# Performance work log

Measured on AMD Instinct MI355X. Metric: run time of the kernel, lower is better.

The kernel has to match this reference:

```python
import jax, jax.numpy as jnp
import numpy as np
from jax.scipy.linalg import solve_triangular

LS = 0.5414            # frozen GP length scale (_gp_scale.data = 0.5414)
L2 = LS * LS
D = 2
K_OPS = D + 2          # operators: identity, d/dx_i (i=1..d), laplacian
JITTER_KXX = 1e-5
JITTER_AKA = 1e-4
JITTER_YY = 1e-5


def _opiK(xout, xin, l2, d):
    # op_i applied to first arg of RBF kernel -> (bs, k, m, n)
    r = xout[:, :, None, :] - xin[:, None, :, :]            # (bs,m,n,d)
    u = jnp.sum(r * r, axis=-1) / l2                        # (bs,m,n)
    K = jnp.exp(-0.5 * u)
    ri = jnp.moveaxis(r, -1, 1)                             # (bs,d,m,n)
    grad = -(ri / l2) * K[:, None]                          # d/dx_i K
    lap = ((u - d) / l2) * K                                # Lap_x K
    return jnp.concatenate([K[:, None], grad, lap[:, None]], axis=1)


def _opiKopjfull(x, l2, d):
    # op_i on first arg, op_j on second arg -> (bs, k, k, m, m)
    r = x[:, :, None, :] - x[:, None, :, :]
    u = jnp.sum(r * r, axis=-1) / l2
    K = jnp.exp(-0.5 * u)
    ri = jnp.moveaxis(r, -1, 1)                             # (bs,d,m,m)
    gK = (ri / l2) * K[:, None]                             # d/dy_j K
    lapK = ((u - d) / l2) * K                               # Lap K (either arg)
    eye = jnp.eye(d, dtype=x.dtype)[None, :, :, None, None]
    gg = (eye / l2 - ri[:, :, None] * ri[:, None] / (l2 * l2)) * K[:, None, None]  # d/dx_i d/dy_j K
    glap = (ri / (l2 * l2)) * (((2.0 + d - u) * K)[:, None])  # d/dx_i Lap_y K
    laplap = (((u - d) ** 2 - 4.0 * u + 2.0 * d) / (l2 * l2)) * K  # Lap_x Lap_y K
    row0 = jnp.concatenate([K[:, None, None], gK[:, None], lapK[:, None, None]], axis=2)
    rowg = jnp.concatenate([(-gK)[:, :, None], gg, glap[:, :, None]], axis=2)
    rowl = jnp.concatenate([lapK[:, None, None], (-glap)[:, None], laplap[:, None, None]], axis=2)
    return jnp.concatenate([row0, rowg, rowl], axis=1)


def _psd_solve(L, B):
    # (Kxx + jitter I)^{-1} B via Cholesky (stands in for gpytorch inv_matmul/CG)
    y = solve_triangular(L, B, lower=True)
    return solve_triangular(L, y, lower=True, trans=1)


def _forward(xin, meanin, Kin, weight, bias):
    bs, n, c = meanin.shape
    d, k, l2 = D, K_OPS, L2
    xout, m = xin, n
    r = xin[:, :, None, :] - xin[:, None, :, :]
    Kxx = jnp.exp(-0.5 * jnp.sum(r * r, axis=-1) / l2)      # (bs,n,n)
    In = jnp.eye(n, dtype=xin.dtype)
    Lc = jnp.linalg.cholesky(Kxx + JITTER_KXX * In)
    opiKmn = _opiK(xout, xin, l2, d)                        # (bs,k,m,n)
    # posterior mean of op_i applied to the GP
    opimean = (opiKmn.reshape(bs, k * m, n) @ _psd_solve(Lc, meanin)).reshape(bs, k, m, c)
    Amean = jnp.transpose(opimean, (0, 2, 3, 1)).reshape(bs, m, c * k) @ weight.T + bias
    W = weight.reshape(-1, c, k)                            # (cout,c,k)
    W2 = jnp.einsum('oci,ocj->ij', W, W) / W.shape[0]       # (k,k)
    Kxxinvopi = jnp.swapaxes(
        _psd_solve(Lc, jnp.swapaxes(opiKmn.reshape(bs, k * m, n), 1, 2)), 1, 2)  # (bs,km,n)
    interp_weights = jnp.swapaxes(_psd_solve(Lc, Kin), 1, 2)                      # (bs,n,n)
    opi_interp = jnp.transpose((Kxxinvopi @ interp_weights).reshape(bs, k, m, n), (0, 2, 3, 1))  # (bs,m,n,k)
    Ak_interp = (opi_interp @ W2).reshape(bs, m, n * k)
    Im = jnp.eye(m, dtype=xin.dtype)
    AkinA = Ak_interp @ jnp.transpose(opiKmn, (0, 3, 1, 2)).reshape(bs, n * k, m) + JITTER_AKA * Im
    opiKxxxopj = jnp.transpose(
        (Kxxinvopi @ jnp.swapaxes(opiKmn.reshape(bs, k * m, n), 1, 2)).reshape(bs, k, m, k, m),
        (0, 1, 3, 2, 4))                                    # (bs,k,k,m,m)
    ijkyy = _opiKopjfull(xout, l2, d) - opiKxxxopj          # posterior cov of op_i f, op_j f
    AkAyy = jnp.einsum('bijmp,ij->bmp', ijkyy, W2) + JITTER_YY * Im
    full_AKA = AkinA + AkAyy
    return (xout, Amean, full_AKA)


def setup_inputs() -> dict:
    bs, n, cin, cout = 4, 576, 32, 64
    key = jax.random.key(0)
    k1, k2, k3, k4, k5 = jax.random.split(key, 5)
    xin = jax.random.uniform(k1, (bs, n, D), dtype=jnp.float32) * 6.0
    meanin = jax.random.normal(k2, (bs, n, cin), dtype=jnp.float32)
    A = jax.random.normal(k3, (bs, n, n), dtype=jnp.float32) / np.float32(np.sqrt(n))
    Kin = A @ jnp.swapaxes(A, 1, 2) + 0.1 * jnp.eye(n, dtype=jnp.float32)  # PSD covariance
    fan_in = cin * K_OPS
    weight = jax.random.normal(k4, (cout, fan_in), dtype=jnp.float32) / np.float32(np.sqrt(fan_in))
    bias = jax.random.normal(k5, (cout,), dtype=jnp.float32) * 0.01
    return {"xin": xin, "meanin": meanin, "Kin": Kin, "weight": weight, "bias": bias}


def reference(xin, meanin, Kin, weight, bias):
    return _forward(xin, meanin, Kin, weight, bias)
```

## Files before the change

kernel.cpp:

```cpp
#include <hip/hip_runtime.h>
#include <math.h>

#define NPTS 576
#define N2 331776
#define BSZ 4
#define NB 64
#define NT 9

#define INVL2 (1.0f/0.29311396f)

typedef __attribute__((ext_vector_type(8))) short short8v;
typedef __attribute__((ext_vector_type(16))) float f32x16;

__global__ void build_k(const float* __restrict__ xin,
                        float* __restrict__ Kxx, float* __restrict__ opiK,
                        float* __restrict__ out,
                        const float* __restrict__ w, float* __restrict__ W2) {
    int idx = blockIdx.x * 256 + threadIdx.x;
    if (idx < 4608) out[idx] = xin[idx];
    int b = idx / N2;
    int rem = idx - b * N2;
    int m = rem / NPTS;
    int nn = rem - m * NPTS;
    const float* xb = xin + (size_t)b * NPTS * 2;
    float xm0 = xb[m*2],  xm1 = xb[m*2+1];
    float xn0 = xb[nn*2], xn1 = xb[nn*2+1];
    float r0 = xm0 - xn0, r1 = xm1 - xn1;
    float u = (r0*r0 + r1*r1) * INVL2;
    float Kv = expf(-0.5f * u);
    Kxx[idx] = Kv + ((m == nn) ? 1e-5f : 0.0f);
    size_t base = (size_t)b * 4 * N2 + rem;
    opiK[base]          = Kv;
    opiK[base + N2]     = -r0 * INVL2 * Kv;
    opiK[base + 2*N2]   = -r1 * INVL2 * Kv;
    opiK[base + 3*N2]   = (u - 2.0f) * INVL2 * Kv;
    if (blockIdx.x == 5183) {
        __shared__ float red[256];
        int tid = threadIdx.x;
        int pair = tid & 15;
        int slice = tid >> 4;
        int i = pair >> 2, j = pair & 3;
        float s = 0.0f;
        for (int o = slice * 4; o < slice * 4 + 4; ++o)
            for (int c = 0; c < 32; ++c)
                s += w[o*128 + c*4 + i] * w[o*128 + c*4 + j];
        red[tid] = s;
        __syncthreads();
        if (tid < 16) {
            float t = 0.0f;
            #pragma unroll
            for (int k = 0; k < 16; ++k) t += red[pair + 16*k];
            W2[pair] = t * (1.0f/64.0f);
        }
    }
}

__device__ void factor_invert_64(float (*T)[NB+1], float (*V)[NB+1],
                                 float (*tmp)[17], int tid) {
    for (int p = 0; p < 4; ++p) {
        int cp = p * 16;
        if (tid < 64) {
            int r = tid;
            float reg[16];
            #pragma unroll
            for (int q = 0; q < 16; ++q) reg[q] = T[r][cp + q];
            #pragma unroll
            for (int j = 0; j < 16; ++j) {
                int col = cp + j;
                float d2 = __shfl(reg[j], col);
                float d = sqrtf(fmaxf(d2, 1e-12f));
                float lr = (r == col) ? d : reg[j] / d;
                reg[j] = lr;
                #pragma unroll
                for (int q = j + 1; q < 16; ++q) {
                    float lc = __shfl(lr, cp + q);
                    if (r >= cp + q) reg[q] -= lr * lc;
                }
            }
            #pragma unroll
            for (int q = 0; q < 16; ++q) T[r][cp + q] = reg[q];
        }
        __syncthreads();
        int tr = 48 - cp;
        if (tr > 0) {
            for (int idx = tid; idx < tr * tr; idx += 256) {
                int r = cp + 16 + idx / tr;
                int c = cp + 16 + idx % tr;
                if (c <= r) {
                    float s = 0.0f;
                    #pragma unroll
                    for (int k = 0; k < 16; ++k) s += T[r][cp+k] * T[c][cp+k];
                    T[r][c] -= s;
                }
            }
        }
        __syncthreads();
    }
    if (tid < 64) {
        int I = tid >> 4, c = tid & 15, base = I * 16;
        float tcol[16];
        #pragma unroll
        for (int i = 0; i < 16; ++i) tcol[i] = T[base + i][base + c];
        float v[16];
        #pragma unroll
        for (int i = 0; i < 16; ++i) {
            float s = (i == c) ? 1.0f : 0.0f;
            #pragma unroll
            for (int k = 0; k < 16; ++k) {
                if (k < i) {
                    float tik = __shfl(tcol[i], base + k);
                    s -= tik * v[k];
                }
            }
            float tii = __shfl(tcol[i], base + i);
            v[i] = s / tii;
        }
        #pragma unroll
        for (int i = 0; i < 16; ++i) V[base + i][base + c] = v[i];
    }
    __syncthreads();
    const int PI[6] = {1,2,3,2,3,3};
    const int PJ[6] = {0,1,2,0,1,0};
    int rr16 = tid >> 4, cc16 = tid & 15;
    for (int p = 0; p < 6; ++p) {
        int I = PI[p], J = PJ[p];
        float s = 0.0f;
        for (int K = J; K < I; ++K)
            #pragma unroll
            for (int t = 0; t < 16; ++t)
                s += T[I*16+rr16][K*16+t] * V[K*16+t][J*16+cc16];
        tmp[rr16][cc16] = s;
        __syncthreads();
        float s2 = 0.0f;
        for (int t = 0; t <= rr16; ++t) s2 += V[I*16+rr16][I*16+t] * tmp[t][cc16];
        __syncthreads();
        V[I*16+rr16][J*16+cc16] = -s2;
        __syncthreads();
    }
}

__global__ void chol_diag0(const float* __restrict__ A, float* __restrict__ LinvKK) {
    int b = blockIdx.x;
    const float* Ab = A + (size_t)b * N2;
    __shared__ float T[NB][NB+1];
    __shared__ float V[NB][NB+1];
    __shared__ float tmp[16][17];
    int tid = threadIdx.x;
    for (int idx = tid; idx < NB*NB; idx += 256) {
        int r = idx >> 6, c = idx & 63;
        T[r][c] = Ab[(size_t)r * NPTS + c];
        V[r][c] = 0.0f;
    }
    __syncthreads();
    factor_invert_64(T, V, tmp, tid);
    float* Vg = LinvKK + (size_t)b * NT * NB * NB;
    for (int idx = tid; idx < NB*NB; idx += 256) Vg[idx] = V[idx >> 6][idx & 63];
}

__global__ __launch_bounds__(256)
void chol_step(float* __restrict__ A, float* __restrict__ LL,
               float* __restrict__ LinvKK, int kb) {
    int b = blockIdx.y;
    int p = blockIdx.x;
    int ir = 0;
    while (p >= ir + 1) { p -= ir + 1; ir++; }
    int ib = kb + 1 + ir, jb = kb + 1 + p;
    float* Ab = A + (size_t)b * N2;
    float* LLb = LL + (size_t)b * N2;
    __shared__ float Ai[NB][NB+1];
    __shared__ float Aj[NB][NB+1];
    __shared__ float Vs[NB][NB+1];
    __shared__ float tmp[16][17];
    int tid = threadIdx.x;
    int tx = tid & 15, ty = tid >> 4;
    const float* Vg = LinvKK + ((size_t)b * NT + kb) * NB * NB;
    bool diag = (ib == jb);
    for (int idx = tid; idx < NB*NB; idx += 256) {
        int r = idx >> 6, c = idx & 63;
        Ai[r][c] = Ab[(size_t)(ib*NB + r) * NPTS + kb*NB + c];
        Aj[r][c] = diag ? 0.0f : Ab[(size_t)(jb*NB + r) * NPTS + kb*NB + c];
        Vs[r][c] = Vg[idx];
    }
    float U[4][4];
    #pragma unroll
    for (int i = 0; i < 4; ++i)
        #pragma unroll
        for (int j = 0; j < 4; ++j)
            U[i][j] = Ab[(size_t)(ib*NB + ty*4+i) * NPTS + jb*NB + tx*4+j];
    __syncthreads();
    float Li[4][4] = {}, Lj[4][4] = {};
    for (int k = 0; k < NB; ++k) {
        float a[4], v[4];
        #pragma unroll
        for (int i = 0; i < 4; ++i) a[i] = Ai[ty*4+i][k];
        #pragma unroll
        for (int j = 0; j < 4; ++j) v[j] = Vs[tx*4+j][k];
        #pragma unroll
        for (int i = 0; i < 4; ++i)
            #pragma unroll
            for (int j = 0; j < 4; ++j) Li[i][j] += a[i] * v[j];
        if (!diag) {
            float aj[4];
            #pragma unroll
            for (int i = 0; i < 4; ++i) aj[i] = Aj[ty*4+i][k];
            #pragma unroll
            for (int i = 0; i < 4; ++i)
                #pragma unroll
                for (int j = 0; j < 4; ++j) Lj[i][j] += aj[i] * v[j];
        }
    }
    __syncthreads();
    #pragma unroll
    for (int i = 0; i < 4; ++i)
        #pragma unroll
        for (int j = 0; j < 4; ++j) {
            Ai[ty*4+i][tx*4+j] = Li[i][j];
            Aj[ty*4+i][tx*4+j] = diag ? Li[i][j] : Lj[i][j];
        }
    if (diag) {
        #pragma unroll
        for (int i = 0; i < 4; ++i)
            #pragma unroll
            for (int j = 0; j < 4; ++j)
                LLb[(size_t)(ib*NB + ty*4+i) * NPTS + kb*NB + tx*4+j] = Li[i][j];
    }
    __syncthreads();
    float s[4][4] = {};
    for (int k = 0; k < NB; ++k) {
        float a[4], v[4];
        #pragma unroll
        for (int i = 0; i < 4; ++i) a[i] = Ai[ty*4+i][k];
        #pragma unroll
        for (int j = 0; j < 4; ++j) v[j] = Aj[tx*4+j][k];
        #pragma unroll
        for (int i = 0; i < 4; ++i)
            #pragma unroll
            for (int j = 0; j < 4; ++j) s[i][j] += a[i] * v[j];
    }
    #pragma unroll
    for (int i = 0; i < 4; ++i)
        #pragma unroll
        for (int j = 0; j < 4; ++j) U[i][j] -= s[i][j];
    if (blockIdx.x != 0) {
        #pragma unroll
        for (int i = 0; i < 4; ++i)
            #pragma unroll
            for (int j = 0; j < 4; ++j)
                Ab[(size_t)(ib*NB + ty*4+i) * NPTS + jb*NB + tx*4+j] = U[i][j];
        return;
    }
    __syncthreads();
    #pragma unroll
    for (int i = 0; i < 4; ++i)
        #pragma unroll
        for (int j = 0; j < 4; ++j) Ai[ty*4+i][tx*4+j] = U[i][j];
    for (int idx = tid; idx < NB*NB; idx += 256) Aj[idx >> 6][idx & 63] = 0.0f;
    __syncthreads();
    factor_invert_64(Ai, Aj, tmp, tid);
    float* Vo = LinvKK + ((size_t)b * NT + (kb + 1)) * NB * NB;
    for (int idx = tid; idx < NB*NB; idx += 256) Vo[idx] = Aj[idx >> 6][idx & 63];
}

__global__ __launch_bounds__(256)
void trinv_blk(const float* __restrict__ L, const float* __restrict__ LinvKK,
               float* __restrict__ Linv) {
    int sp = blockIdx.x, jb = blockIdx.y, b = blockIdx.z;
    const float* Lb = L + (size_t)b * N2;
    float* Xg = Linv + (size_t)b * N2;
    const float* Vg = LinvKK + (size_t)b * NT * NB * NB;
    int c0 = jb * NB + sp * 16;

    __shared__ float LsT[64][72];
    __shared__ float Xc[576][17];
    __shared__ float Ss[64][17];

    int tid = threadIdx.x;
    int tx = tid & 15, ty = tid >> 4;
    int sr = tid >> 2, st0 = (tid & 3) * 16;

    float4 pf0, pf1, pf2, pf3;

#define TRINV_ISSUE_L(ibv, kbv)                                               \
    { const float* src_ = Lb + (size_t)((ibv) * NB + sr) * NPTS + (kbv) * NB + st0; \
      pf0 = *(const float4*)(src_ + 0);  pf1 = *(const float4*)(src_ + 4);    \
      pf2 = *(const float4*)(src_ + 8);  pf3 = *(const float4*)(src_ + 12); }

#define TRINV_ISSUE_V(ibv)                                                    \
    { const float* src_ = Vg + (size_t)(ibv) * NB * NB + sr * NB + st0;       \
      pf0 = *(const float4*)(src_ + 0);  pf1 = *(const float4*)(src_ + 4);    \
      pf2 = *(const float4*)(src_ + 8);  pf3 = *(const float4*)(src_ + 12); }

#define TRINV_COMMIT()                                                        \
    { LsT[st0 + 0][sr]  = pf0.x; LsT[st0 + 1][sr]  = pf0.y;                   \
      LsT[st0 + 2][sr]  = pf0.z; LsT[st0 + 3][sr]  = pf0.w;                   \
      LsT[st0 + 4][sr]  = pf1.x; LsT[st0 + 5][sr]  = pf1.y;                   \
      LsT[st0 + 6][sr]  = pf1.z; LsT[st0 + 7][sr]  = pf1.w;                   \
      LsT[st0 + 8][sr]  = pf2.x; LsT[st0 + 9][sr]  = pf2.y;                   \
      LsT[st0 + 10][sr] = pf2.z; LsT[st0 + 11][sr] = pf2.w;                   \
      LsT[st0 + 12][sr] = pf3.x; LsT[st0 + 13][sr] = pf3.y;                   \
      LsT[st0 + 14][sr] = pf3.z; LsT[st0 + 15][sr] = pf3.w; }

    {
        const float* Vjj = Vg + (size_t)jb * NB * NB;
        int r = tid >> 2, c4 = (tid & 3) * 4;
        float4 v = *(const float4*)(Vjj + r * NB + sp * 16 + c4);
        Xc[r][c4+0] = v.x; Xc[r][c4+1] = v.y; Xc[r][c4+2] = v.z; Xc[r][c4+3] = v.w;
        *(float4*)(Xg + (size_t)(jb * NB + r) * NPTS + c0 + c4) = v;
    }
    if (jb + 1 < NT) TRINV_ISSUE_L(jb + 1, jb);
    __syncthreads();

    for (int ib = jb + 1; ib < NT; ++ib) {
        float acc[4] = {};
        for (int kb = jb; kb < ib; ++kb) {
            TRINV_COMMIT();
            __syncthreads();
            if (kb + 1 < ib) { TRINV_ISSUE_L(ib, kb + 1); }
            else             { TRINV_ISSUE_V(ib); }
            int xbase = (kb - jb) * 64;
            #pragma unroll 8
            for (int t = 0; t < 64; ++t) {
                float a4[4]; *(float4*)a4 = *(const float4*)&LsT[t][ty*4];
                float xv = Xc[xbase + t][tx];
                #pragma unroll
                for (int i = 0; i < 4; ++i) acc[i] += a4[i] * xv;
            }
            __syncthreads();
        }
        TRINV_COMMIT();
        #pragma unroll
        for (int i = 0; i < 4; ++i) Ss[ty*4+i][tx] = acc[i];
        __syncthreads();
        if (ib + 1 < NT) TRINV_ISSUE_L(ib + 1, jb);
        float acc2[4] = {};
        #pragma unroll 8
        for (int t = 0; t < 64; ++t) {
            float a4[4]; *(float4*)a4 = *(const float4*)&LsT[t][ty*4];
            float sv = Ss[t][tx];
            #pragma unroll
            for (int i = 0; i < 4; ++i) acc2[i] += a4[i] * sv;
        }
        int obase = (ib - jb) * 64;
        #pragma unroll
        for (int i = 0; i < 4; ++i) {
            float v = -acc2[i];
            Xc[obase + ty*4 + i][tx] = v;
            Xg[(size_t)(ib * NB + ty*4 + i) * NPTS + c0 + tx] = v;
        }
        __syncthreads();
    }
#undef TRINV_ISSUE_L
#undef TRINV_ISSUE_V
#undef TRINV_COMMIT
}

__device__ inline void split3(float v, unsigned short& h0, unsigned short& h1,
                              unsigned short& h2) {
    unsigned u0 = __float_as_uint(v) & 0xffff0000u;
    float f0 = __uint_as_float(u0);
    float r1 = v - f0;
    unsigned u1 = __float_as_uint(r1) & 0xffff0000u;
    float f1 = __uint_as_float(u1);
    float r2 = r1 - f1;
    h0 = (unsigned short)(u0 >> 16);
    h1 = (unsigned short)(u1 >> 16);
    h2 = (unsigned short)((__float_as_uint(r2) + 0x8000u) >> 16);
}

__device__ inline void pack_store(unsigned short* dst, const unsigned short* v) {
    uint4 w;
    w.x = (unsigned)v[0] | ((unsigned)v[1] << 16);
    w.y = (unsigned)v[2] | ((unsigned)v[3] << 16);
    w.z = (unsigned)v[4] | ((unsigned)v[5] << 16);
    w.w = (unsigned)v[6] | ((unsigned)v[7] << 16);
    *(uint4*)dst = w;
}

template<int EPIB>
__global__ __launch_bounds__(256, 2)
void mm_p2_mfma(const float* __restrict__ Aall, const float* __restrict__ Ball,
                float* __restrict__ Call, long sA, long sB, long sC)
{
    int id = blockIdx.x;
    int x8 = id & 7, qq = id >> 3;
    int nx = qq % 9;
    int band = x8 + 8 * (qq / 9);
    if (band >= 18 * BSZ) return;
    int t  = band % 18;
    int b  = band / 18;
    int pp = t / 9, my = t % 9;
    const float* A0 = Aall + (size_t)b * sA + (size_t)(pp * 2) * N2;
    const float* A1 = A0 + N2;
    const float* B  = Ball + (size_t)b * sB;
    float* C0 = Call + (size_t)b * sC + (size_t)(pp * 2) * N2;
    float* C1 = C0 + N2;
    int n0 = nx * 64, m0 = my * 64;

    __shared__ __align__(16) unsigned short As[12][2][64][8];
    __shared__ __align__(16) unsigned short Bs[6][2][64][8];

    int tid  = threadIdx.x;
    int lane = tid & 63;
    int wid  = tid >> 6;
    int wr = wid >> 1, wc = wid & 1;

    f32x16 acc0, acc1;
    #pragma unroll
    for (int i = 0; i < 16; ++i) { acc0[i] = 0.0f; acc1[i] = 0.0f; }

    int ap   = tid >> 7;
    int aq   = tid & 127;
    int ar   = aq >> 1;
    int asub = aq & 1;
    const float* Apl = ap ? A1 : A0;
    int areg = ar >> 5;
    int aln  = ar & 31;

    int bc   = tid & 63;
    int bkg  = tid >> 6;
    int bsub = bkg >> 1;
    int bln  = (bc & 31) + 32 * (bkg & 1);
    int bwc  = bc >> 5;

    float av[16];
    float bv[8];

    auto loadA = [&](int k0) {
        const float* p = Apl + (size_t)(m0 + ar) * 576 + k0 + asub * 16;
        float4 t0 = *(const float4*)(p);
        float4 t1 = *(const float4*)(p + 4);
        float4 t2 = *(const float4*)(p + 8);
        float4 t3 = *(const float4*)(p + 12);
        av[0]=t0.x;  av[1]=t0.y;  av[2]=t0.z;  av[3]=t0.w;
        av[4]=t1.x;  av[5]=t1.y;  av[6]=t1.z;  av[7]=t1.w;
        av[8]=t2.x;  av[9]=t2.y;  av[10]=t2.z; av[11]=t2.w;
        av[12]=t3.x; av[13]=t3.y; av[14]=t3.z; av[15]=t3.w;
    };
    auto loadB = [&](int k0) {
        const float* p = B + (size_t)(k0 + bkg * 8) * 576 + n0 + bc;
        #pragma unroll
        for (int j = 0; j < 8; ++j) {
            float v = p[(size_t)j * 576];
            if (EPIB) { if (k0 + bkg * 8 + j == n0 + bc) v -= 1.0f; }
            bv[j] = v;
        }
    };
    auto storeA = [&]() {
        unsigned short s0[16], s1[16], s2[16];
        #pragma unroll
        for (int j = 0; j < 16; ++j) split3(av[j], s0[j], s1[j], s2[j]);
        #pragma unroll
        for (int h = 0; h < 2; ++h) {
            int ln = aln + 32 * h;
            pack_store(&As[(ap*3 + 0)*2 + areg][asub][ln][0], &s0[8*h]);
            pack_store(&As[(ap*3 + 1)*2 + areg][asub][ln][0], &s1[8*h]);
            pack_store(&As[(ap*3 + 2)*2 + areg][asub][ln][0], &s2[8*h]);
        }
    };
    auto storeB = [&]() {
        unsigned short s0[8], s1[8], s2[8];
        #pragma unroll
        for (int j = 0; j < 8; ++j) split3(bv[j], s0[j], s1[j], s2[j]);
        pack_store(&Bs[0*2 + bwc][bsub][bln][0], s0);
        pack_store(&Bs[1*2 + bwc][bsub][bln][0], s1);
        pack_store(&Bs[2*2 + bwc][bsub][bln][0], s2);
    };

    const short8v* Af = (const short8v*)As;
    const short8v* Bf = (const short8v*)Bs;

    loadA(0); loadB(0);
    for (int k0 = 0; k0 < 576; k0 += 32) {
        storeA(); storeB();
        __syncthreads();
        if (k0 + 32 < 576) { loadA(k0 + 32); loadB(k0 + 32); }
        #pragma unroll
        for (int sub = 0; sub < 2; ++sub) {
            short8v b0 = Bf[((0*2 + wc)*2 + sub)*64 + lane];
            short8v b1 = Bf[((1*2 + wc)*2 + sub)*64 + lane];
            short8v b2 = Bf[((2*2 + wc)*2 + sub)*64 + lane];
            short8v a0 = Af[((0*3 + 0)*2 + wr)*128 + sub*64 + lane];
            short8v a1 = Af[((0*3 + 1)*2 + wr)*128 + sub*64 + lane];
            short8v a2 = Af[((0*3 + 2)*2 + wr)*128 + sub*64 + lane];
            acc0 = __builtin_amdgcn_mfma_f32_32x32x16_bf16(a0, b0, acc0, 0, 0, 0);
            acc0 = __builtin_amdgcn_mfma_f32_32x32x16_bf16(a0, b1, acc0, 0, 0, 0);
            acc0 = __builtin_amdgcn_mfma_f32_32x32x16_bf16(a1, b0, acc0, 0, 0, 0);
            acc0 = __builtin_amdgcn_mfma_f32_32x32x16_bf16(a1, b1, acc0, 0, 0, 0);
            acc0 = __builtin_amdgcn_mfma_f32_32x32x16_bf16(a0, b2, acc0, 0, 0, 0);
            acc0 = __builtin_amdgcn_mfma_f32_32x32x16_bf16(a2, b0, acc0, 0, 0, 0);
            a0 = Af[((1*3 + 0)*2 + wr)*128 + sub*64 + lane];
            a1 = Af[((1*3 + 1)*2 + wr)*128 + sub*64 + lane];
            a2 = Af[((1*3 + 2)*2 + wr)*128 + sub*64 + lane];
            acc1 = __builtin_amdgcn_mfma_f32_32x32x16_bf16(a0, b0, acc1, 0, 0, 0);
            acc1 = __builtin_amdgcn_mfma_f32_32x32x16_bf16(a0, b1, acc1, 0, 0, 0);
            acc1 = __builtin_amdgcn_mfma_f32_32x32x16_bf16(a1, b0, acc1, 0, 0, 0);
            acc1 = __builtin_amdgcn_mfma_f32_32x32x16_bf16(a1, b1, acc1, 0, 0, 0);
            acc1 = __builtin_amdgcn_mfma_f32_32x32x16_bf16(a0, b2, acc1, 0, 0, 0);
            acc1 = __builtin_amdgcn_mfma_f32_32x32x16_bf16(a2, b0, acc1, 0, 0, 0);
        }
        __syncthreads();
    }

    int colg = n0 + 32*wc + (lane & 31);
    int rowb = m0 + 32*wr + 4*(lane >> 5);
    #pragma unroll
    for (int reg = 0; reg < 16; ++reg) {
        int row = rowb + (reg & 3) + 8*(reg >> 2);
        C0[(size_t)row * 576 + colg] = acc0[reg];
        C1[(size_t)row * 576 + colg] = acc1[reg];
    }
}

__global__ __launch_bounds__(256, 2)
void mm_abt_mfma(const float* __restrict__ Aall, const float* __restrict__ Ball,
                 float* __restrict__ Call, long sA, long sB, long sC, long sSplit)
{
    int p = blockIdx.x;
    int ir = 0;
    while (p >= ir + 1) { p -= ir + 1; ir++; }
    int my = ir, nx = p;
    int zz = blockIdx.z;
    int sp = zz & 3, b = zz >> 2;
    const float* A = Aall + (size_t)b * sA + (size_t)sp * N2;
    const float* B = Ball + (size_t)b * sB + (size_t)sp * N2;
    float* Cp = Call + (size_t)b * sC + (size_t)sp * sSplit;
    int m0 = my * 64, n0 = nx * 64;

    __shared__ __align__(16) unsigned short Fr[12][2][64][8];

    int tid  = threadIdx.x;
    int lane = tid & 63;
    int wid  = tid >> 6;
    int wr = wid >> 1, wc = wid & 1;

    f32x16 acc;
    #pragma unroll
    for (int i = 0; i < 16; ++i) acc[i] = 0.0f;

    int sel  = tid >> 7;
    int q2   = tid & 127;
    int r    = q2 >> 1;
    int ssub = q2 & 1;
    const float* Src = sel ? B : A;
    int base0 = sel ? n0 : m0;
    int rreg = r >> 5;
    int rln  = r & 31;

    float av[16];

    auto loadF = [&](int k0) {
        const float* pp = Src + (size_t)(base0 + r) * 576 + k0 + ssub * 16;
        float4 t0 = *(const float4*)(pp);
        float4 t1 = *(const float4*)(pp + 4);
        float4 t2 = *(const float4*)(pp + 8);
        float4 t3 = *(const float4*)(pp + 12);
        av[0]=t0.x;  av[1]=t0.y;  av[2]=t0.z;  av[3]=t0.w;
        av[4]=t1.x;  av[5]=t1.y;  av[6]=t1.z;  av[7]=t1.w;
        av[8]=t2.x;  av[9]=t2.y;  av[10]=t2.z; av[11]=t2.w;
        av[12]=t3.x; av[13]=t3.y; av[14]=t3.z; av[15]=t3.w;
    };
    auto storeF = [&]() {
        unsigned short s0[16], s1[16], s2[16];
        #pragma unroll
        for (int j = 0; j < 16; ++j) split3(av[j], s0[j], s1[j], s2[j]);
        #pragma unroll
        for (int h = 0; h < 2; ++h) {
            int ln = rln + 32 * h;
            pack_store(&Fr[sel*6 + 0*2 + rreg][ssub][ln][0], &s0[8*h]);
            pack_store(&Fr[sel*6 + 1*2 + rreg][ssub][ln][0], &s1[8*h]);
            pack_store(&Fr[sel*6 + 2*2 + rreg][ssub][ln][0], &s2[8*h]);
        }
    };

    const short8v* Ff = (const short8v*)Fr;

    loadF(0);
    for (int k0 = 0; k0 < 576; k0 += 32) {
        storeF();
        __syncthreads();
        if (k0 + 32 < 576) loadF(k0 + 32);
        #pragma unroll
        for (int sub = 0; sub < 2; ++sub) {
            short8v a0 = Ff[((0*2 + wr)*2 + sub)*64 + lane];
            short8v a1 = Ff[((1*2 + wr)*2 + sub)*64 + lane];
            short8v a2 = Ff[((2*2 + wr)*2 + sub)*64 + lane];
            short8v b0 = Ff[((6 + 0*2 + wc)*2 + sub)*64 + lane];
            short8v b1 = Ff[((6 + 1*2 + wc)*2 + sub)*64 + lane];
            short8v b2 = Ff[((6 + 2*2 + wc)*2 + sub)*64 + lane];
            acc = __builtin_amdgcn_mfma_f32_32x32x16_bf16(a0, b0, acc, 0, 0, 0);
            acc = __builtin_amdgcn_mfma_f32_32x32x16_bf16(a0, b1, acc, 0, 0, 0);
            acc = __builtin_amdgcn_mfma_f32_32x32x16_bf16(a1, b0, acc, 0, 0, 0);
            acc = __builtin_amdgcn_mfma_f32_32x32x16_bf16(a1, b1, acc, 0, 0, 0);
            acc = __builtin_amdgcn_mfma_f32_32x32x16_bf16(a0, b2, acc, 0, 0, 0);
            acc = __builtin_amdgcn_mfma_f32_32x32x16_bf16(a2, b0, acc, 0, 0, 0);
        }
        __syncthreads();
    }

    int colg = n0 + 32*wc + (lane & 31);
    int rowb = m0 + 32*wr + 4*(lane >> 5);
    #pragma unroll
    for (int reg = 0; reg < 16; ++reg) {
        int row = rowb + (reg & 3) + 8*(reg >> 2);
        Cp[(size_t)row * 576 + colg] = acc[reg];
    }
}

__global__ __launch_bounds__(256, 2)
void mm_ata_mfma(const float* __restrict__ Lg, float* __restrict__ C,
                 long sA, long sC)
{
    int p = blockIdx.x;
    int ir = 0;
    while (p >= ir + 1) { p -= ir + 1; ir++; }
    int my = ir, nx = p;
    int b = blockIdx.z;
    const float* A = Lg + (size_t)b * sA;
    float* Cb = C + (size_t)b * sC;
    int m0 = my * 64, n0 = nx * 64;
    int kBeg = m0;

    __shared__ __align__(16) unsigned short Fr[12][2][64][8];

    int tid  = threadIdx.x;
    int lane = tid & 63;
    int wid  = tid >> 6;
    int wr = wid >> 1, wc = wid & 1;

    f32x16 acc;
    #pragma unroll
    for (int i = 0; i < 16; ++i) acc[i] = 0.0f;

    int sel  = tid >> 7;
    int q2   = tid & 127;
    int col  = q2 & 63;
    int ssub = q2 >> 6;
    int c0base = sel ? n0 : m0;
    int rreg = col >> 5;
    int rln  = col & 31;

    float av[16];

    auto loadF = [&](int k0) {
        const float* pp = A + (size_t)(k0 + ssub * 16) * 576 + c0base + col;
        #pragma unroll
        for (int j = 0; j < 16; ++j) av[j] = pp[(size_t)j * 576];
    };
    auto storeF = [&]() {
        unsigned short s0[16], s1[16], s2[16];
        #pragma unroll
        for (int j = 0; j < 16; ++j) split3(av[j], s0[j], s1[j], s2[j]);
        #pragma unroll
        for (int h = 0; h < 2; ++h) {
            int ln = rln + 32 * h;
            pack_store(&Fr[sel*6 + 0*2 + rreg][ssub][ln][0], &s0[8*h]);
            pack_store(&Fr[sel*6 + 1*2 + rreg][ssub][ln][0], &s1[8*h]);
            pack_store(&Fr[sel*6 + 2*2 + rreg][ssub][ln][0], &s2[8*h]);
        }
    };

    const short8v* Ff = (const short8v*)Fr;

    loadF(kBeg);
    for (int k0 = kBeg; k0 < 576; k0 += 32) {
        storeF();
        __syncthreads();
        if (k0 + 32 < 576) loadF(k0 + 32);
        #pragma unroll
        for (int sub = 0; sub < 2; ++sub) {
            short8v a0 = Ff[((0*2 + wr)*2 + sub)*64 + lane];
            short8v a1 = Ff[((1*2 + wr)*2 + sub)*64 + lane];
            short8v a2 = Ff[((2*2 + wr)*2 + sub)*64 + lane];
            short8v b0 = Ff[((6 + 0*2 + wc)*2 + sub)*64 + lane];
            short8v b1 = Ff[((6 + 1*2 + wc)*2 + sub)*64 + lane];
            short8v b2 = Ff[((6 + 2*2 + wc)*2 + sub)*64 + lane];
            acc = __builtin_amdgcn_mfma_f32_32x32x16_bf16(a0, b0, acc, 0, 0, 0);
            acc = __builtin_amdgcn_mfma_f32_32x32x16_bf16(a0, b1, acc, 0, 0, 0);
            acc = __builtin_amdgcn_mfma_f32_32x32x16_bf16(a1, b0, acc, 0, 0, 0);
            acc = __builtin_amdgcn_mfma_f32_32x32x16_bf16(a1, b1, acc, 0, 0, 0);
            acc = __builtin_amdgcn_mfma_f32_32x32x16_bf16(a0, b2, acc, 0, 0, 0);
            acc = __builtin_amdgcn_mfma_f32_32x32x16_bf16(a2, b0, acc, 0, 0, 0);
        }
        __syncthreads();
    }

    int colg = n0 + 32*wc + (lane & 31);
    int rowb = m0 + 32*wr + 4*(lane >> 5);
    #pragma unroll
    for (int reg = 0; reg < 16; ++reg) {
        int row = rowb + (reg & 3) + 8*(reg >> 2);
        float v = acc[reg];
        Cb[(size_t)row * 576 + colg] = v;
        Cb[(size_t)colg * 576 + row] = v;
    }
}

__global__ __launch_bounds__(256, 2)
void mm_ab_mfma(const float* __restrict__ Aall, const float* __restrict__ Ball,
                float* __restrict__ Call, long sA, long sB, long sC)
{
    int nx = blockIdx.x % 9, my = blockIdx.x / 9;
    int b = blockIdx.z;
    const float* A = Aall + (size_t)b * sA;
    const float* B = Ball + (size_t)b * sB;
    float* Cb = Call + (size_t)b * sC;
    int m0 = my * 64, n0 = nx * 64;

    __shared__ __align__(16) unsigned short Fr[12][2][64][8];

    int tid  = threadIdx.x;
    int lane = tid & 63;
    int wid  = tid >> 6;
    int wr = wid >> 1, wc = wid & 1;

    f32x16 acc;
    #pragma unroll
    for (int i = 0; i < 16; ++i) acc[i] = 0.0f;

    int sel  = tid >> 7;
    int q2   = tid & 127;
    int ar   = q2 >> 1;
    int asub = q2 & 1;
    int areg = ar >> 5, aln = ar & 31;
    int bcol = q2 & 63;
    int bssub = q2 >> 6;
    int breg = bcol >> 5, brln = bcol & 31;

    float av[16];

    auto loadF = [&](int k0) {
        if (sel == 0) {
            const float* pp = A + (size_t)(m0 + ar) * 576 + k0 + asub * 16;
            float4 t0 = *(const float4*)(pp);
            float4 t1 = *(const float4*)(pp + 4);
            float4 t2 = *(const float4*)(pp + 8);
            float4 t3 = *(const float4*)(pp + 12);
            av[0]=t0.x;  av[1]=t0.y;  av[2]=t0.z;  av[3]=t0.w;
            av[4]=t1.x;  av[5]=t1.y;  av[6]=t1.z;  av[7]=t1.w;
            av[8]=t2.x;  av[9]=t2.y;  av[10]=t2.z; av[11]=t2.w;
            av[12]=t3.x; av[13]=t3.y; av[14]=t3.z; av[15]=t3.w;
        } else {
            const float* pp = B + (size_t)(k0 + bssub * 16) * 576 + n0 + bcol;
            #pragma unroll
            for (int j = 0; j < 16; ++j) av[j] = pp[(size_t)j * 576];
        }
    };
    auto storeF = [&]() {
        unsigned short s0[16], s1[16], s2[16];
        #pragma unroll
        for (int j = 0; j < 16; ++j) split3(av[j], s0[j], s1[j], s2[j]);
        int reg0 = sel ? (6 + 0*2 + breg) : (0*2 + areg);
        int reg1 = sel ? (6 + 1*2 + breg) : (1*2 + areg);
        int reg2 = sel ? (6 + 2*2 + breg) : (2*2 + areg);
        int sb   = sel ? bssub : asub;
        int ln0  = sel ? brln : aln;
        #pragma unroll
        for (int h = 0; h < 2; ++h) {
            int ln = ln0 + 32 * h;
            pack_store(&Fr[reg0][sb][ln][0], &s0[8*h]);
            pack_store(&Fr[reg1][sb][ln][0], &s1[8*h]);
            pack_store(&Fr[reg2][sb][ln][0], &s2[8*h]);
        }
    };

    const short8v* Ff = (const short8v*)Fr;

    loadF(0);
    for (int k0 = 0; k0 < 576; k0 += 32) {
        storeF();
        __syncthreads();
        if (k0 + 32 < 576) loadF(k0 + 32);
        #pragma unroll
        for (int sub = 0; sub < 2; ++sub) {
            short8v a0 = Ff[((0*2 + wr)*2 + sub)*64 + lane];
            short8v a1 = Ff[((1*2 + wr)*2 + sub)*64 + lane];
            short8v a2 = Ff[((2*2 + wr)*2 + sub)*64 + lane];
            short8v b0 = Ff[((6 + 0*2 + wc)*2 + sub)*64 + lane];
            short8v b1 = Ff[((6 + 1*2 + wc)*2 + sub)*64 + lane];
            short8v b2 = Ff[((6 + 2*2 + wc)*2 + sub)*64 + lane];
            acc = __builtin_amdgcn_mfma_f32_32x32x16_bf16(a0, b0, acc, 0, 0, 0);
            acc = __builtin_amdgcn_mfma_f32_32x32x16_bf16(a0, b1, acc, 0, 0, 0);
            acc = __builtin_amdgcn_mfma_f32_32x32x16_bf16(a1, b0, acc, 0, 0, 0);
            acc = __builtin_amdgcn_mfma_f32_32x32x16_bf16(a1, b1, acc, 0, 0, 0);
            acc = __builtin_amdgcn_mfma_f32_32x32x16_bf16(a0, b2, acc, 0, 0, 0);
            acc = __builtin_amdgcn_mfma_f32_32x32x16_bf16(a2, b0, acc, 0, 0, 0);
        }
        __syncthreads();
    }

    int colg = n0 + 32*wc + (lane & 31);
    int rowb = m0 + 32*wr + 4*(lane >> 5);
    #pragma unroll
    for (int reg = 0; reg < 16; ++reg) {
        int row = rowb + (reg & 3) + 8*(reg >> 2);
        Cb[(size_t)row * 576 + colg] = acc[reg];
    }
}

template<int TA, int TB, int SK, int TRI, int SWZ, int EPIB, int TRIC>
__global__ __launch_bounds__(256)
void mm_kernel(const float* __restrict__ Aall, const float* __restrict__ Ball,
               float* __restrict__ Call,
               int M, int N, int K, int planeK,
               int lda, int ldb, int ldc,
               long sA, long sB, long sC, long pA, long pB, long sSplit, int MT)
{
    int nx, my, zz;
    if (TRIC) {
        int p = blockIdx.x;
        int ir = 0;
        while (p >= ir + 1) { p -= ir + 1; ir++; }
        my = ir; nx = p; zz = blockIdx.z;
    } else if (SWZ) {
        int id = blockIdx.x;
        int x8 = id & 7;
        int q  = id >> 3;
        nx = q % 9;
        int band = x8 + 8 * (q / 9);
        if (band >= MT * 4 * SK) return;
        my = band % MT;
        zz = band / MT;
    } else { nx = blockIdx.x; my = blockIdx.y; zz = blockIdx.z; }
    int sp = (SK > 1) ? (zz % SK) : 0;
    int b  = (SK > 1) ? (zz / SK) : zz;
    const float* A = Aall + (size_t)b * sA;
    const float* B = Ball + (size_t)b * sB;
    float* C = Call + (size_t)b * sC + (size_t)sp * sSplit;
    int n0 = nx * 64;
    int m0 = my * 64;

    __shared__ float As[16][68];
    __shared__ float Bs[16][68];

    int tid = threadIdx.x;
    int tx = tid & 15, ty = tid >> 4;

    float acc[4][4] = {};
    bool mFull = (m0 + 64 <= M);
    bool nFull = (n0 + 64 <= N);

    int triBeg = 0;
    if (TRI) { int mx = (m0 > n0 ? m0 : n0); triBeg = mx & ~15; }
    int kBeg = triBeg, kEnd = K;
    if (SK > 1) {
        int len = K - triBeg;
        int chunk = ((len / SK) + 15) & ~15;
        kBeg = triBeg + sp * chunk;
        if (kBeg > K) kBeg = K;
        kEnd = (sp == SK - 1) ? K : (kBeg + chunk < K ? kBeg + chunk : K);
    }

    float avr[4];
    float bvr[4];

    auto loadA = [&](int k0) {
        int plane = k0 / planeK;
        int koff  = k0 - plane * planeK;
        if (TA == 0) {
            const float* Ab = A + (size_t)pA * plane;
            int r = tid >> 2, c4 = (tid & 3) * 4;
            int gm = m0 + r;
            if (mFull || gm < M) {
                float4 t = *(const float4*)(Ab + (size_t)gm * lda + koff + c4);
                avr[0]=t.x; avr[1]=t.y; avr[2]=t.z; avr[3]=t.w;
            } else { avr[0]=avr[1]=avr[2]=avr[3]=0.0f; }
        } else {
            int r = tid >> 4, c4 = (tid & 15) * 4;
            const float* p = A + (size_t)(koff + r) * lda + m0 + c4;
            if (mFull) {
                float4 t = *(const float4*)p;
                avr[0]=t.x; avr[1]=t.y; avr[2]=t.z; avr[3]=t.w;
            } else {
                #pragma unroll
                for (int jj = 0; jj < 4; ++jj)
                    avr[jj] = (m0 + c4 + jj < M) ? p[jj] : 0.0f;
            }
        }
    };
    auto storeA = [&]() {
        if (TA == 0) {
            int r = tid >> 2, c4 = (tid & 3) * 4;
            #pragma unroll
            for (int q = 0; q < 4; ++q) As[c4+q][r] = avr[q];
        } else {
            int r = tid >> 4, c4 = (tid & 15) * 4;
            #pragma unroll
            for (int q = 0; q < 4; ++q) As[r][c4+q] = avr[q];
        }
    };
    auto loadB = [&](int k0) {
        int plane = k0 / planeK;
        int koff  = k0 - plane * planeK;
        if (TB == 0) {
            int r = tid >> 4, c4 = (tid & 15) * 4;
            const float* p = B + (size_t)(koff + r) * ldb + n0 + c4;
            if (nFull) {
                float4 t = *(const float4*)p;
                bvr[0]=t.x; bvr[1]=t.y; bvr[2]=t.z; bvr[3]=t.w;
            } else {
                #pragma unroll
                for (int jj = 0; jj < 4; ++jj)
                    bvr[jj] = (n0 + c4 + jj < N) ? p[jj] : 0.0f;
            }
            if (EPIB) {
                int gk = koff + r;
                #pragma unroll
                for (int jj = 0; jj < 4; ++jj)
                    if (gk == n0 + c4 + jj) bvr[jj] -= 1.0f;
            }
        } else {
            const float* Bb = B + (size_t)pB * plane;
            int r = tid >> 2, c4 = (tid & 3) * 4;
            int gp = n0 + r;
            if (nFull || gp < N) {
                float4 t = *(const float4*)(Bb + (size_t)gp * ldb + koff + c4);
                bvr[0]=t.x; bvr[1]=t.y; bvr[2]=t.z; bvr[3]=t.w;
            } else { bvr[0]=bvr[1]=bvr[2]=bvr[3]=0.0f; }
        }
    };
    auto storeB = [&]() {
        if (TB == 0) {
            int r = tid >> 4, c4 = (tid & 15) * 4;
            #pragma unroll
            for (int q = 0; q < 4; ++q) Bs[r][c4+q] = bvr[q];
        } else {
            int r = tid >> 2, c4 = (tid & 3) * 4;
            #pragma unroll
            for (int q = 0; q < 4; ++q) Bs[c4+q][r] = bvr[q];
        }
    };

    if (kBeg < kEnd) {
        loadA(kBeg); loadB(kBeg);
        for (int k0 = kBeg; k0 < kEnd; k0 += 16) {
            storeA(); storeB();
            __syncthreads();
            if (k0 + 16 < kEnd) { loadA(k0 + 16); loadB(k0 + 16); }
            #pragma unroll
            for (int kk = 0; kk < 16; ++kk) {
                float a[4], bb[4];
                *(float4*)a  = *(const float4*)&As[kk][ty*4];
                *(float4*)bb = *(const float4*)&Bs[kk][tx*4];
                #pragma unroll
                for (int i = 0; i < 4; ++i)
                    #pragma unroll
                    for (int j = 0; j < 4; ++j)
                        acc[i][j] += a[i] * bb[j];
            }
            __syncthreads();
        }
    }

    #pragma unroll
    for (int i = 0; i < 4; ++i) {
        int gm = m0 + ty*4 + i;
        if (gm >= M) continue;
        #pragma unroll
        for (int j = 0; j < 4; ++j) {
            int gn = n0 + tx*4 + j;
            if (gn >= N) continue;
            C[(size_t)gm * ldc + gn] = acc[i][j];
        }
    }
}

__global__ void combine_solm4(const float* __restrict__ p, float* __restrict__ o) {
    int i = blockIdx.x * 256 + threadIdx.x;
    o[i] = p[i] + p[i + 73728] + p[i + 2*73728] + p[i + 3*73728];
}

__global__ void combine_prior4_sym(const float* __restrict__ p0,
                                   const float* __restrict__ xin,
                                   const float* __restrict__ W2g,
                                   float* __restrict__ o, long stride) {
    __shared__ float w[16];
    int tid = threadIdx.x;
    if (tid < 16) w[tid] = W2g[tid];
    __syncthreads();
    int idx = blockIdx.x * 256 + tid;
    int b = idx / N2;
    int rem = idx - b * N2;
    int m = rem / NPTS, n = rem - m * NPTS;
    if (m < n) return;
    const float* xb = xin + (size_t)b * NPTS * 2;
    float r0 = xb[m*2+0] - xb[n*2+0];
    float r1 = xb[m*2+1] - xb[n*2+1];
    float u = (r0*r0 + r1*r1) * INVL2;
    float Kv = expf(-0.5f * u);
    float i2 = INVL2 * INVL2;
    float gK0 = r0 * INVL2 * Kv;
    float gK1 = r1 * INVL2 * Kv;
    float lapK = (u - 2.0f) * INVL2 * Kv;
    float gg00 = (INVL2 - r0*r0*i2) * Kv;
    float gg01 = (-r0*r1*i2) * Kv;
    float gg11 = (INVL2 - r1*r1*i2) * Kv;
    float gl0 = r0 * i2 * (4.0f - u) * Kv;
    float gl1 = r1 * i2 * (4.0f - u) * Kv;
    float ll = ((u-2.0f)*(u-2.0f) - 4.0f*u + 4.0f) * i2 * Kv;
    float prior =
          w[0]*Kv + w[1]*gK0 + w[2]*gK1 + w[3]*lapK
        + w[4]*(-gK0) + w[5]*gg00 + w[6]*gg01 + w[7]*gl0
        + w[8]*(-gK1) + w[9]*gg01 + w[10]*gg11 + w[11]*gl1
        + w[12]*lapK + w[13]*(-gl0) + w[14]*(-gl1) + w[15]*ll;
    float v = p0[idx] + p0[idx + stride] + p0[idx + 2*stride] + p0[idx + 3*stride]
            + prior;
    if (m == n) v += 1.1e-4f;
    o[(size_t)b * N2 + (size_t)m * NPTS + n] = v;
    if (m != n)
        o[(size_t)b * N2 + (size_t)n * NPTS + m] = v;
}

__global__ void opiw2_k(const float* __restrict__ opiK, const float* __restrict__ W2,
                        float* __restrict__ outB) {
    int idx = blockIdx.x * 256 + threadIdx.x;
    int b = idx / N2;
    int rem = idx - b * N2;
    size_t base = (size_t)b * 4 * N2 + rem;
    float k0 = opiK[base], k1 = opiK[base + N2], k2 = opiK[base + 2*N2], k3 = opiK[base + 3*N2];
    #pragma unroll
    for (int i = 0; i < 4; ++i)
        outB[base + (size_t)i * N2] = W2[i*4+0]*k0 + W2[i*4+1]*k1 + W2[i*4+2]*k2 + W2[i*4+3]*k3;
}

__global__ __launch_bounds__(256)
void amean_k(const float* __restrict__ opimean, const float* __restrict__ weight,
             const float* __restrict__ bias, float* __restrict__ out) {
    int b = blockIdx.y;
    int m0 = blockIdx.x * 32;
    __shared__ float Wl[64][128];
    __shared__ float om[32][128];
    int tid = threadIdx.x;
    for (int idx = tid; idx < 64*128; idx += 256) Wl[idx / 128][idx & 127] = weight[idx];
    for (int idx = tid; idx < 32*128; idx += 256) {
        int m = idx >> 7, ck = idx & 127, c = ck >> 2, kop = ck & 3;
        om[m][ck] = opimean[((size_t)b * 4 + kop) * NPTS * 32 + (size_t)(m0 + m) * 32 + c];
    }
    __syncthreads();
    int ml = tid >> 3, o0 = (tid & 7) * 8;
    float acc[8] = {};
    for (int ck = 0; ck < 128; ++ck) {
        float v = om[ml][ck];
        #pragma unroll
        for (int q = 0; q < 8; ++q) acc[q] += v * Wl[o0+q][ck];
    }
    #pragma unroll
    for (int q = 0; q < 8; ++q)
        out[4608 + ((size_t)b * NPTS + m0 + ml) * 64 + o0 + q] = acc[q] + bias[o0+q];
}

static inline int gridSwz(int MT, int Z) { return 8 * 9 * ((MT * Z + 7) / 8); }

extern "C" void kernel_launch(void* const* d_in, const int* in_sizes, int n_in,
                              void* d_out, int out_size, void* d_ws, size_t ws_size,
                              hipStream_t stream) {
    const float* xin    = (const float*)d_in[0];
    const float* meanin = (const float*)d_in[1];
    const float* Kin    = (const float*)d_in[2];
    const float* weight = (const float*)d_in[3];
    const float* bias   = (const float*)d_in[4];
    float* out = (float*)d_out;
    float* ws  = (float*)d_ws;

    const long N2L = N2;
    float* W2      = ws;
    float* LinvKK  = ws + 64;
    float* R1 = LinvKK + 147456;
    float* R2 = R1 + 4*N2L;
    float* R3 = R2 + 4*N2L;
    float* R4 = R3 + 4*N2L;
    float* R5 = R4 + 16*N2L;
    float* R6 = R5 + 16*N2L;

    hipMemsetAsync(R2, 0, (size_t)4 * N2 * sizeof(float), stream);
    build_k<<<dim3((BSZ*N2)/256), dim3(256), 0, stream>>>(
        xin, R1, R4, out, weight, W2);
    chol_diag0<<<dim3(BSZ), dim3(256), 0, stream>>>(R1, LinvKK);
    for (int kb = 0; kb < NT - 1; ++kb) {
        int t = NT - 1 - kb;
        chol_step<<<dim3(t*(t+1)/2, BSZ), dim3(256), 0, stream>>>(R1, R3, LinvKK, kb);
    }
    trinv_blk<<<dim3(4, NT, BSZ), dim3(256), 0, stream>>>(R3, LinvKK, R2);
    mm_ata_mfma<<<dim3(45, 1, BSZ), dim3(256), 0, stream>>>(R2, R3, N2L, N2L);
    mm_kernel<0,0,4,0,0,0,0><<<dim3(1,9,16), dim3(256), 0, stream>>>(
        R3, meanin, R6, 576,32,576,576, 576,32,32,
        N2L,18432,18432, 0,0, 73728, 9);
    combine_solm4<<<dim3(288), dim3(256), 0, stream>>>(R6, R2);
    mm_kernel<0,0,1,0,0,0,0><<<dim3(1,36,BSZ), dim3(256), 0, stream>>>(
        R4, R2, R2 + 73728, 2304,32,576,576, 576,32,32,
        4*N2L,18432,73728, 0,0, 0, 9);
    amean_k<<<dim3(18,BSZ), dim3(256), 0, stream>>>(R2 + 73728, weight, bias, out);
    mm_ab_mfma<<<dim3(81, 1, BSZ), dim3(256), 0, stream>>>(
        Kin, R3, R1, N2L, N2L, N2L);
    mm_p2_mfma<0><<<dim3(gridSwz(18,4)), dim3(256), 0, stream>>>(
        R4, R3, R5, 4*N2L, N2L, 4*N2L);
    opiw2_k<<<dim3((BSZ*N2)/256), dim3(256), 0, stream>>>(R4, W2, R4);
    mm_p2_mfma<1><<<dim3(gridSwz(18,4)), dim3(256), 0, stream>>>(
        R5, R1, R6, 4*N2L, N2L, 4*N2L);
    mm_abt_mfma<<<dim3(45,1,BSZ*4), dim3(256), 0, stream>>>(
        R6, R4, R5, 4*N2L, 4*N2L, N2L, 4*N2L);
    combine_prior4_sym<<<dim3(5184), dim3(256), 0, stream>>>(
        R5, xin, W2, out + 152064, 4*N2L);
}
```

Measured before the change: 874.5 us.

## Use split-K 4x4 register tiles with shared-memory reduction in trinv_blk

```diff
diff --git a/kernel.cpp b/kernel.cpp
--- a/kernel.cpp
+++ b/kernel.cpp
@@ -271,11 +271,14 @@
     int c0 = jb * NB + sp * 16;
 
     __shared__ float LsT[64][72];
-    __shared__ float Xc[576][17];
-    __shared__ float Ss[64][17];
+    __shared__ float Xc[576][20];
+    __shared__ float Ss[64][20];
+    __shared__ float Red[4][64][20];
 
     int tid = threadIdx.x;
-    int tx = tid & 15, ty = tid >> 4;
+    int kq = tid >> 6;
+    int rg = (tid >> 2) & 15;
+    int cg = tid & 3;
     int sr = tid >> 2, st0 = (tid & 3) * 16;
 
     float4 pf0, pf1, pf2, pf3;
@@ -304,48 +307,82 @@
         const float* Vjj = Vg + (size_t)jb * NB * NB;
         int r = tid >> 2, c4 = (tid & 3) * 4;
         float4 v = *(const float4*)(Vjj + r * NB + sp * 16 + c4);
-        Xc[r][c4+0] = v.x; Xc[r][c4+1] = v.y; Xc[r][c4+2] = v.z; Xc[r][c4+3] = v.w;
+        *(float4*)&Xc[r][c4] = v;
         *(float4*)(Xg + (size_t)(jb * NB + r) * NPTS + c0 + c4) = v;
     }
     if (jb + 1 < NT) TRINV_ISSUE_L(jb + 1, jb);
     __syncthreads();
 
     for (int ib = jb + 1; ib < NT; ++ib) {
-        float acc[4] = {};
+        float acc[4][4] = {};
         for (int kb = jb; kb < ib; ++kb) {
             TRINV_COMMIT();
             __syncthreads();
             if (kb + 1 < ib) { TRINV_ISSUE_L(ib, kb + 1); }
             else             { TRINV_ISSUE_V(ib); }
             int xbase = (kb - jb) * 64;
-            #pragma unroll 8
-            for (int t = 0; t < 64; ++t) {
-                float a4[4]; *(float4*)a4 = *(const float4*)&LsT[t][ty*4];
-                float xv = Xc[xbase + t][tx];
+            #pragma unroll
+            for (int t = 0; t < 16; ++t) {
+                int k = kq * 16 + t;
+                float a4[4]; *(float4*)a4 = *(const float4*)&LsT[k][rg * 4];
+                float x4[4]; *(float4*)x4 = *(const float4*)&Xc[xbase + k][cg * 4];
                 #pragma unroll
-                for (int i = 0; i < 4; ++i) acc[i] += a4[i] * xv;
+                for (int i = 0; i < 4; ++i)
+                    #pragma unroll
+                    for (int j = 0; j < 4; ++j)
+                        acc[i][j] += a4[i] * x4[j];
             }
             __syncthreads();
         }
         TRINV_COMMIT();
         #pragma unroll
-        for (int i = 0; i < 4; ++i) Ss[ty*4+i][tx] = acc[i];
+        for (int i = 0; i < 4; ++i)
+            *(float4*)&Red[kq][rg * 4 + i][cg * 4] = *(float4*)&acc[i][0];
+        __syncthreads();
+        {
+            int r = tid >> 2, c4 = (tid & 3) * 4;
+            float4 s0 = *(float4*)&Red[0][r][c4];
+            float4 s1 = *(float4*)&Red[1][r][c4];
+            float4 s2 = *(float4*)&Red[2][r][c4];
+            float4 s3 = *(float4*)&Red[3][r][c4];
+            float4 s; s.x = s0.x + s1.x + s2.x + s3.x;
+            s.y = s0.y + s1.y + s2.y + s3.y;
+            s.z = s0.z + s1.z + s2.z + s3.z;
+            s.w = s0.w + s1.w + s2.w + s3.w;
+            *(float4*)&Ss[r][c4] = s;
+        }
         __syncthreads();
         if (ib + 1 < NT) TRINV_ISSUE_L(ib + 1, jb);
-        float acc2[4] = {};
-        #pragma unroll 8
-        for (int t = 0; t < 64; ++t) {
-            float a4[4]; *(float4*)a4 = *(const float4*)&LsT[t][ty*4];
-            float sv = Ss[t][tx];
-            #pragma unroll
-            for (int i = 0; i < 4; ++i) acc2[i] += a4[i] * sv;
-        }
+        float acc2[4][4] = {};
+        #pragma unroll
+        for (int t = 0; t < 16; ++t) {
+            int k = kq * 16 + t;
+            float a4[4]; *(float4*)a4 = *(const float4*)&LsT[k][rg * 4];
+            float s4[4]; *(float4*)s4 = *(const float4*)&Ss[k][cg * 4];
+            #pragma unroll
+            for (int i = 0; i < 4; ++i)
+                #pragma unroll
+                for (int j = 0; j < 4; ++j)
+                    acc2[i][j] += a4[i] * s4[j];
+        }
+        __syncthreads();
+        #pragma unroll
+        for (int i = 0; i < 4; ++i)
+            *(float4*)&Red[kq][rg * 4 + i][cg * 4] = *(float4*)&acc2[i][0];
+        __syncthreads();
         int obase = (ib - jb) * 64;
-        #pragma unroll
-        for (int i = 0; i < 4; ++i) {
-            float v = -acc2[i];
-            Xc[obase + ty*4 + i][tx] = v;
-            Xg[(size_t)(ib * NB + ty*4 + i) * NPTS + c0 + tx] = v;
+        {
+            int r = tid >> 2, c4 = (tid & 3) * 4;
+            float4 s0 = *(float4*)&Red[0][r][c4];
+            float4 s1 = *(float4*)&Red[1][r][c4];
+            float4 s2 = *(float4*)&Red[2][r][c4];
+            float4 s3 = *(float4*)&Red[3][r][c4];
+            float4 s; s.x = -(s0.x + s1.x + s2.x + s3.x);
+            s.y = -(s0.y + s1.y + s2.y + s3.y);
+            s.z = -(s0.z + s1.z + s2.z + s3.z);
+            s.w = -(s0.w + s1.w + s2.w + s3.w);
+            *(float4*)&Xc[obase + r][c4] = s;
+            *(float4*)(Xg + (size_t)(ib * NB + r) * NPTS + c0 + c4) = s;
         }
         __syncthreads();
     }
```

Result: no change. 857.9 us, median of 2 (-1.9%).
